# Kernel optimization log

Measured on AMD Instinct MI355X. Metric: run time of the kernel, lower is better.

Reference implementation:

```python
import jax, jax.numpy as jnp
import numpy as np

N_NODES = 50000

def _gcn_norm(edge_index, num_nodes):
    # add self-loops, compute symmetric normalization D^-1/2 (A+I) D^-1/2
    loops = jnp.arange(num_nodes, dtype=edge_index.dtype)
    row = jnp.concatenate([edge_index[0], loops])  # target nodes
    col = jnp.concatenate([edge_index[1], loops])  # source nodes
    deg = jax.ops.segment_sum(jnp.ones_like(row, dtype=jnp.float32), row, num_segments=num_nodes)
    dinv = jnp.where(deg > 0, 1.0 / jnp.sqrt(deg), 0.0)
    norm = dinv[row] * dinv[col]  # [E+N]
    return row, col, norm

def _gcn_layer(x, W, b, row, col, norm, num_nodes):
    h = x @ W  # [N, out] transform first (PyG GCNConv order)
    msg = h[col] * norm[:, None]  # gather sources, scale
    out = jax.ops.segment_sum(msg, row, num_segments=num_nodes)  # scatter-add to targets
    return out + b

def setup_inputs() -> dict:
    key = jax.random.key(0)
    ks = jax.random.split(key, 8)
    F_IN, HID, C = 512, 128, 40
    x = jax.random.normal(ks[0], (N_NODES, F_IN), dtype=jnp.float32)
    edge_index = jax.random.randint(ks[1], (2, 800000), 0, N_NODES, dtype=jnp.int32)
    W1 = jax.random.normal(ks[2], (F_IN, HID), dtype=jnp.float32) / np.sqrt(F_IN)
    b1 = jnp.zeros((HID,), dtype=jnp.float32)
    W2 = jax.random.normal(ks[3], (HID, HID), dtype=jnp.float32) / np.sqrt(HID)
    b2 = jnp.zeros((HID,), dtype=jnp.float32)
    W3 = jax.random.normal(ks[4], (HID, C), dtype=jnp.float32) / np.sqrt(HID)
    b3 = jnp.zeros((C,), dtype=jnp.float32)
    return {"x": x, "edge_index": edge_index, "W1": W1, "b1": b1, "W2": W2, "b2": b2, "W3": W3, "b3": b3}

def reference(x, edge_index, W1, b1, W2, b2, W3, b3):
    row, col, norm = _gcn_norm(edge_index, N_NODES)
    h = _gcn_layer(x, W1, b1, row, col, norm, N_NODES)
    h = jax.nn.relu(h)  # dropout is identity in eval mode
    h = _gcn_layer(h, W2, b2, row, col, norm, N_NODES)
    h = jax.nn.relu(h)
    h = _gcn_layer(h, W3, b3, row, col, norm, N_NODES)
    return jax.nn.log_softmax(h, axis=1)
```

## Files before the change

kernel.cpp:

```cpp
#include <hip/hip_runtime.h>
#include <hip/hip_bf16.h>
#include <math.h>

#define N_NODES 50000
#define N_EDGES 800000
#define F_IN 512
#define HID 128
#define NCLS 40
#define CAP 64
#define NBIN 8
#define BIN_SZ 6250

typedef unsigned short u16;
typedef __attribute__((ext_vector_type(8))) short short8;
typedef __attribute__((ext_vector_type(4))) float f32x4;

__device__ inline u16 f2bf(float f) {
    unsigned int u = __float_as_uint(f);
    unsigned int r = (u + 0x7FFFu + ((u >> 16) & 1u)) >> 16;
    return (u16)r;
}
__device__ inline float bf2f(u16 b) {
    return __uint_as_float(((unsigned int)b) << 16);
}


__global__ void k_zero_cnt(int* __restrict__ cnt) {
    int i = blockIdx.x * 256 + threadIdx.x;
    if (i < N_NODES) cnt[i] = 0;
}

__global__ void k_scatter_fx(const int* __restrict__ row, const int* __restrict__ col,
                             int* __restrict__ cnt, int* __restrict__ csr_col) {
    int bin = blockIdx.x & 7;
    int gblk = blockIdx.x >> 3;
    int nblk = gridDim.x >> 3;
    int lo = bin * BIN_SZ, hi = lo + BIN_SZ;
    for (int e = gblk * 256 + threadIdx.x; e < N_EDGES; e += nblk * 256) {
        int r = row[e];
        if (r >= lo && r < hi) {
            int pos = atomicAdd(&cnt[r], 1);
            if (pos < CAP) csr_col[(size_t)r * CAP + pos] = col[e];
        }
    }
}

__global__ void k_dinv_fx(int* __restrict__ cnt, float* __restrict__ dinv) {
    int i = blockIdx.x * 256 + threadIdx.x;
    if (i < N_NODES) {
        int d = cnt[i];
        if (d > CAP) { d = CAP; cnt[i] = CAP; }
        dinv[i] = rsqrtf((float)(d + 1));
    }
}

__global__ void k_nrm_fx(const int* __restrict__ cnt, const int* __restrict__ csr_col,
                         const float* __restrict__ dinv, float* __restrict__ csr_nrm) {
    int gid = blockIdx.x * 256 + threadIdx.x;
    if (gid >= N_NODES * CAP) return;
    int i = gid >> 6;
    int s = gid & (CAP - 1);
    if (s < cnt[i]) {
        int c = csr_col[(size_t)i * CAP + s];
        csr_nrm[(size_t)i * CAP + s] = dinv[i] * dinv[c];
    }
}


__global__ void k_wsplit(const float* __restrict__ W, u16* __restrict__ Whi, int Kdim) {
    int idx = blockIdx.x * 256 + threadIdx.x;
    if (idx >= Kdim * 128) return;
    int k = idx >> 7, n = idx & 127;
    u16 hb = f2bf(W[idx]);
    int s = k >> 5, hq = (k >> 3) & 3, q = k & 7;
    int j = n >> 4, lnn = n & 15;
    size_t pos = ((((size_t)s * 8 + j) * 16 + lnn) * 32) + hq * 8 + q;
    Whi[pos] = hb;
}


template<int K, bool AF32>
__device__ __forceinline__ void gemm_body(const void* __restrict__ Ap,
                                          const u16* __restrict__ Wh,
                                          u16* __restrict__ C, int M) {
    constexpr int NC = K / 64;
    constexpr int CH_BYTES = AF32 ? 8192 : 4096;
    __shared__ unsigned char sA[2][CH_BYTES];

    const int t = threadIdx.x;
    const int w = t >> 6, l = t & 63;
    const int ln = l & 15, h = l >> 4;
    const int row0 = blockIdx.x * 32;

    f32x4 acc[2][2];
    #pragma unroll
    for (int i = 0; i < 2; ++i)
        #pragma unroll
        for (int jj = 0; jj < 2; ++jj)
            acc[i][jj] = (f32x4){0.f, 0.f, 0.f, 0.f};

    auto stage = [&](int c, int buf) {
        if constexpr (AF32) {
            const float* X = (const float*)Ap;
            #pragma unroll
            for (int i = 0; i < 2; ++i) {
                int f = i * 256 + t;
                int r = f >> 4;
                int sub = f & 15;
                int srow = row0 + r; if (srow > M - 1) srow = M - 1;
                int colf = (sub * 4) ^ ((r & 7) << 3);
                const float* gp = X + (size_t)srow * K + c * 64 + colf;
                unsigned char* lp = &sA[buf][f * 16];
                __builtin_amdgcn_global_load_lds(
                    (const __attribute__((address_space(1))) void*)gp,
                    (__attribute__((address_space(3))) void*)lp, 16, 0, 0);
            }
        } else {
            const u16* X = (const u16*)Ap;
            int r = t >> 3;
            int sub = t & 7;
            int srow = row0 + r; if (srow > M - 1) srow = M - 1;
            int cole = (sub * 8) ^ ((r & 7) << 3);
            const u16* gp = X + (size_t)srow * K + c * 64 + cole;
            unsigned char* lp = &sA[buf][t * 16];
            __builtin_amdgcn_global_load_lds(
                (const __attribute__((address_space(1))) void*)gp,
                (__attribute__((address_space(3))) void*)lp, 16, 0, 0);
        }
    };

    stage(0, 0);
    __syncthreads();

    int buf = 0;
    for (int c = 0; c < NC; ++c) {
        short8 bh[2][2];
        #pragma unroll
        for (int s = 0; s < 2; ++s) {
            const int sg = c * 2 + s;
            #pragma unroll
            for (int jj = 0; jj < 2; ++jj) {
                size_t off = ((((size_t)sg * 8 + 2 * w + jj) * 16 + ln) * 32) + h * 8;
                bh[s][jj] = *(const short8*)(Wh + off);
            }
        }
        if (c + 1 < NC) stage(c + 1, buf ^ 1);

        short8 ah[2][2];
        if constexpr (AF32) {
            #pragma unroll
            for (int s = 0; s < 2; ++s)
                #pragma unroll
                for (int i = 0; i < 2; ++i) {
                    int rb = (i * 16 + ln) * 256;
                    int sw = (ln & 7) << 5;
                    int a0 = rb + ((s * 128 + h * 32) ^ sw);
                    float4 p0 = *(const float4*)&sA[buf][a0];
                    float4 p1 = *(const float4*)&sA[buf][a0 + 16];
                    union { short8 s8; u16 u[8]; } cv;
                    cv.u[0] = f2bf(p0.x); cv.u[1] = f2bf(p0.y);
                    cv.u[2] = f2bf(p0.z); cv.u[3] = f2bf(p0.w);
                    cv.u[4] = f2bf(p1.x); cv.u[5] = f2bf(p1.y);
                    cv.u[6] = f2bf(p1.z); cv.u[7] = f2bf(p1.w);
                    ah[s][i] = cv.s8;
                }
        } else {
            #pragma unroll
            for (int s = 0; s < 2; ++s)
                #pragma unroll
                for (int i = 0; i < 2; ++i) {
                    int rb = (i * 16 + ln) * 128;
                    int sw = (ln & 7) << 4;
                    ah[s][i] = *(const short8*)&sA[buf][rb + ((s * 64 + h * 16) ^ sw)];
                }
        }

        #pragma unroll
        for (int s = 0; s < 2; ++s)
            #pragma unroll
            for (int i = 0; i < 2; ++i)
                #pragma unroll
                for (int jj = 0; jj < 2; ++jj)
                    acc[i][jj] = __builtin_amdgcn_mfma_f32_16x16x32_bf16(
                        ah[s][i], bh[s][jj], acc[i][jj], 0, 0, 0);

        __syncthreads();
        buf ^= 1;
    }

    #pragma unroll
    for (int i = 0; i < 2; ++i)
        #pragma unroll
        for (int v = 0; v < 4; ++v) {
            int gr = row0 + i * 16 + h * 4 + v;
            if (gr < M) {
                #pragma unroll
                for (int jj = 0; jj < 2; ++jj)
                    __builtin_nontemporal_store(
                        f2bf(acc[i][jj][v]),
                        &C[(size_t)gr * 128 + w * 32 + jj * 16 + ln]);
            }
        }
}

__global__ __launch_bounds__(256) void k_gemmL1(const void* __restrict__ Ap,
                                                const u16* __restrict__ Wh,
                                                u16* __restrict__ C, int M) {
    gemm_body<F_IN, true>(Ap, Wh, C, M);
}

__global__ __launch_bounds__(256) void k_gemmL2(const void* __restrict__ Ap,
                                                const u16* __restrict__ Wh,
                                                u16* __restrict__ C, int M) {
    gemm_body<HID, false>(Ap, Wh, C, M);
}


__global__ void k_gemm40(const u16* __restrict__ A, const float* __restrict__ W,
                         u16* __restrict__ C, int M) {
    __shared__ float As[64][132];
    __shared__ float Ws[128][40];
    int t = threadIdx.x;
    int row0 = blockIdx.x * 64;
    #pragma unroll
    for (int i = 0; i < 4; ++i) {
        int fidx = t + i * 256;
        int r = fidx >> 4;
        int c = (fidx & 15) * 8;
        int gr = row0 + r;
        uint4 v = {0, 0, 0, 0};
        if (gr < M) v = *reinterpret_cast<const uint4*>(A + (size_t)gr * 128 + c);
        const u16* pv = (const u16*)&v;
        #pragma unroll
        for (int q = 0; q < 8; ++q) As[r][c + q] = bf2f(pv[q]);
    }
    #pragma unroll
    for (int i = 0; i < 5; ++i) {
        int fidx = t + i * 256;
        int r = fidx / 10, c = (fidx % 10) << 2;
        float4 v = *reinterpret_cast<const float4*>(W + r * 40 + c);
        *reinterpret_cast<float4*>(&Ws[r][c]) = v;
    }
    __syncthreads();
    int r = t >> 2;
    int cg = t & 3;
    float acc[10];
    #pragma unroll
    for (int j = 0; j < 10; ++j) acc[j] = 0.0f;
    for (int k = 0; k < 128; ++k) {
        float a = As[r][k];
        #pragma unroll
        for (int j = 0; j < 10; ++j)
            acc[j] = fmaf(a, Ws[k][cg * 10 + j], acc[j]);
    }
    int gr = row0 + r;
    if (gr < M) {
        u16* base = C + (size_t)gr * 40 + cg * 10;
        #pragma unroll
        for (int j = 0; j < 5; ++j) {
            unsigned int p = (unsigned int)f2bf(acc[2 * j]) |
                             ((unsigned int)f2bf(acc[2 * j + 1]) << 16);
            __builtin_nontemporal_store(p, (unsigned int*)(base + 2 * j));
        }
    }
}


__global__ void k_agg_csr_bf(const u16* __restrict__ h, const float* __restrict__ dinv,
                             const float* __restrict__ bias,
                             const int* __restrict__ cnt, const int* __restrict__ csr_col,
                             const float* __restrict__ csr_nrm, u16* __restrict__ out) {
    int gid = blockIdx.x * 256 + threadIdx.x;
    if (gid >= N_NODES * 32) return;
    int i = gid >> 5;
    int q = (gid & 31) * 4;
    const u16* hq = h + q;
    float di = dinv[i];
    float s = di * di;
    ushort4 hv = *reinterpret_cast<const ushort4*>(hq + (size_t)i * 128);
    float4 bv = *reinterpret_cast<const float4*>(bias + q);
    float4 acc;
    acc.x = fmaf(bf2f(hv.x), s, bv.x);
    acc.y = fmaf(bf2f(hv.y), s, bv.y);
    acc.z = fmaf(bf2f(hv.z), s, bv.z);
    acc.w = fmaf(bf2f(hv.w), s, bv.w);
    int e = (int)((size_t)i * CAP);
    int e1 = e + cnt[i];
    for (; e + 8 <= e1; e += 8) {
        int c0 = csr_col[e],     c1 = csr_col[e + 1], c2 = csr_col[e + 2], c3 = csr_col[e + 3];
        int c4 = csr_col[e + 4], c5 = csr_col[e + 5], c6 = csr_col[e + 6], c7 = csr_col[e + 7];
        float n0 = csr_nrm[e],     n1 = csr_nrm[e + 1], n2 = csr_nrm[e + 2], n3 = csr_nrm[e + 3];
        float n4 = csr_nrm[e + 4], n5 = csr_nrm[e + 5], n6 = csr_nrm[e + 6], n7 = csr_nrm[e + 7];
        ushort4 v0 = *reinterpret_cast<const ushort4*>(hq + (size_t)c0 * 128);
        ushort4 v1 = *reinterpret_cast<const ushort4*>(hq + (size_t)c1 * 128);
        ushort4 v2 = *reinterpret_cast<const ushort4*>(hq + (size_t)c2 * 128);
        ushort4 v3 = *reinterpret_cast<const ushort4*>(hq + (size_t)c3 * 128);
        ushort4 v4 = *reinterpret_cast<const ushort4*>(hq + (size_t)c4 * 128);
        ushort4 v5 = *reinterpret_cast<const ushort4*>(hq + (size_t)c5 * 128);
        ushort4 v6 = *reinterpret_cast<const ushort4*>(hq + (size_t)c6 * 128);
        ushort4 v7 = *reinterpret_cast<const ushort4*>(hq + (size_t)c7 * 128);
        acc.x = fmaf(bf2f(v0.x), n0, acc.x); acc.y = fmaf(bf2f(v0.y), n0, acc.y);
        acc.z = fmaf(bf2f(v0.z), n0, acc.z); acc.w = fmaf(bf2f(v0.w), n0, acc.w);
        acc.x = fmaf(bf2f(v1.x), n1, acc.x); acc.y = fmaf(bf2f(v1.y), n1, acc.y);
        acc.z = fmaf(bf2f(v1.z), n1, acc.z); acc.w = fmaf(bf2f(v1.w), n1, acc.w);
        acc.x = fmaf(bf2f(v2.x), n2, acc.x); acc.y = fmaf(bf2f(v2.y), n2, acc.y);
        acc.z = fmaf(bf2f(v2.z), n2, acc.z); acc.w = fmaf(bf2f(v2.w), n2, acc.w);
        acc.x = fmaf(bf2f(v3.x), n3, acc.x); acc.y = fmaf(bf2f(v3.y), n3, acc.y);
        acc.z = fmaf(bf2f(v3.z), n3, acc.z); acc.w = fmaf(bf2f(v3.w), n3, acc.w);
        acc.x = fmaf(bf2f(v4.x), n4, acc.x); acc.y = fmaf(bf2f(v4.y), n4, acc.y);
        acc.z = fmaf(bf2f(v4.z), n4, acc.z); acc.w = fmaf(bf2f(v4.w), n4, acc.w);
        acc.x = fmaf(bf2f(v5.x), n5, acc.x); acc.y = fmaf(bf2f(v5.y), n5, acc.y);
        acc.z = fmaf(bf2f(v5.z), n5, acc.z); acc.w = fmaf(bf2f(v5.w), n5, acc.w);
        acc.x = fmaf(bf2f(v6.x), n6, acc.x); acc.y = fmaf(bf2f(v6.y), n6, acc.y);
        acc.z = fmaf(bf2f(v6.z), n6, acc.z); acc.w = fmaf(bf2f(v6.w), n6, acc.w);
        acc.x = fmaf(bf2f(v7.x), n7, acc.x); acc.y = fmaf(bf2f(v7.y), n7, acc.y);
        acc.z = fmaf(bf2f(v7.z), n7, acc.z); acc.w = fmaf(bf2f(v7.w), n7, acc.w);
    }
    for (; e < e1; ++e) {
        int c0 = csr_col[e];
        float n0 = csr_nrm[e];
        ushort4 v0 = *reinterpret_cast<const ushort4*>(hq + (size_t)c0 * 128);
        acc.x = fmaf(bf2f(v0.x), n0, acc.x); acc.y = fmaf(bf2f(v0.y), n0, acc.y);
        acc.z = fmaf(bf2f(v0.z), n0, acc.z); acc.w = fmaf(bf2f(v0.w), n0, acc.w);
    }
    ushort4 o;
    o.x = f2bf(fmaxf(acc.x, 0.f));
    o.y = f2bf(fmaxf(acc.y, 0.f));
    o.z = f2bf(fmaxf(acc.z, 0.f));
    o.w = f2bf(fmaxf(acc.w, 0.f));
    *reinterpret_cast<ushort4*>(out + (size_t)i * 128 + q) = o;
}


__global__ void k_agg_csr40_bf(const u16* __restrict__ h, const float* __restrict__ dinv,
                               const float* __restrict__ bias,
                               const int* __restrict__ cnt, const int* __restrict__ csr_col,
                               const float* __restrict__ csr_nrm, float* __restrict__ out) {
    const int TPN = 10;
    int gid = blockIdx.x * 256 + threadIdx.x;
    if (gid >= N_NODES * TPN) return;
    int i = gid / TPN;
    int q = (gid % TPN) * 4;
    const u16* hq = h + q;
    float di = dinv[i];
    float s = di * di;
    ushort4 hv = *reinterpret_cast<const ushort4*>(hq + (size_t)i * 40);
    float4 bv = *reinterpret_cast<const float4*>(bias + q);
    float4 acc;
    acc.x = fmaf(bf2f(hv.x), s, bv.x);
    acc.y = fmaf(bf2f(hv.y), s, bv.y);
    acc.z = fmaf(bf2f(hv.z), s, bv.z);
    acc.w = fmaf(bf2f(hv.w), s, bv.w);
    int e = (int)((size_t)i * CAP);
    int e1 = e + cnt[i];
    for (; e + 4 <= e1; e += 4) {
        int c0 = csr_col[e], c1 = csr_col[e + 1], c2 = csr_col[e + 2], c3 = csr_col[e + 3];
        float n0 = csr_nrm[e], n1 = csr_nrm[e + 1], n2 = csr_nrm[e + 2], n3 = csr_nrm[e + 3];
        ushort4 v0 = *reinterpret_cast<const ushort4*>(hq + (size_t)c0 * 40);
        ushort4 v1 = *reinterpret_cast<const ushort4*>(hq + (size_t)c1 * 40);
        ushort4 v2 = *reinterpret_cast<const ushort4*>(hq + (size_t)c2 * 40);
        ushort4 v3 = *reinterpret_cast<const ushort4*>(hq + (size_t)c3 * 40);
        acc.x = fmaf(bf2f(v0.x), n0, acc.x); acc.y = fmaf(bf2f(v0.y), n0, acc.y);
        acc.z = fmaf(bf2f(v0.z), n0, acc.z); acc.w = fmaf(bf2f(v0.w), n0, acc.w);
        acc.x = fmaf(bf2f(v1.x), n1, acc.x); acc.y = fmaf(bf2f(v1.y), n1, acc.y);
        acc.z = fmaf(bf2f(v1.z), n1, acc.z); acc.w = fmaf(bf2f(v1.w), n1, acc.w);
        acc.x = fmaf(bf2f(v2.x), n2, acc.x); acc.y = fmaf(bf2f(v2.y), n2, acc.y);
        acc.z = fmaf(bf2f(v2.z), n2, acc.z); acc.w = fmaf(bf2f(v2.w), n2, acc.w);
        acc.x = fmaf(bf2f(v3.x), n3, acc.x); acc.y = fmaf(bf2f(v3.y), n3, acc.y);
        acc.z = fmaf(bf2f(v3.z), n3, acc.z); acc.w = fmaf(bf2f(v3.w), n3, acc.w);
    }
    for (; e < e1; ++e) {
        int c0 = csr_col[e];
        float n0 = csr_nrm[e];
        ushort4 v0 = *reinterpret_cast<const ushort4*>(hq + (size_t)c0 * 40);
        acc.x = fmaf(bf2f(v0.x), n0, acc.x); acc.y = fmaf(bf2f(v0.y), n0, acc.y);
        acc.z = fmaf(bf2f(v0.z), n0, acc.z); acc.w = fmaf(bf2f(v0.w), n0, acc.w);
    }
    *reinterpret_cast<float4*>(out + (size_t)i * 40 + q) = acc;
}


__global__ void k_logsoftmax(float* __restrict__ out) {
    int wave = threadIdx.x >> 6, lane = threadIdx.x & 63;
    int rowi = blockIdx.x * 4 + wave;
    if (rowi >= N_NODES) return;
    float v = (lane < NCLS) ? out[(size_t)rowi * NCLS + lane] : -INFINITY;
    float m = v;
    #pragma unroll
    for (int off = 32; off; off >>= 1) m = fmaxf(m, __shfl_xor(m, off));
    float ex = (lane < NCLS) ? expf(v - m) : 0.0f;
    float s = ex;
    #pragma unroll
    for (int off = 32; off; off >>= 1) s += __shfl_xor(s, off);
    float ls = logf(s);
    if (lane < NCLS) out[(size_t)rowi * NCLS + lane] = v - m - ls;
}


extern "C" void kernel_launch(void* const* d_in, const int* in_sizes, int n_in,
                              void* d_out, int out_size, void* d_ws, size_t ws_size,
                              hipStream_t stream) {
    const float* x  = (const float*)d_in[0];
    const int* ei   = (const int*)d_in[1];
    const float* W1 = (const float*)d_in[2];
    const float* b1 = (const float*)d_in[3];
    const float* W2 = (const float*)d_in[4];
    const float* b2 = (const float*)d_in[5];
    const float* W3 = (const float*)d_in[6];
    const float* b3 = (const float*)d_in[7];
    float* out = (float*)d_out;

    const int* row = ei;
    const int* col = ei + N_EDGES;

    char* ws = (char*)d_ws;
    int*   cnt     = (int*)ws;   ws += sizeof(int) * N_NODES;
    int*   csr_col = (int*)ws;   ws += sizeof(int) * (size_t)N_NODES * CAP;
    float* csr_nrm = (float*)ws; ws += sizeof(float) * (size_t)N_NODES * CAP;
    float* dinv    = (float*)ws; ws += sizeof(float) * N_NODES;
    u16*   wt1hi   = (u16*)ws;   ws += sizeof(u16) * F_IN * 128;
    u16*   wt2hi   = (u16*)ws;   ws += sizeof(u16) * HID * 128;
    u16*   hbuf    = (u16*)ws;   ws += sizeof(u16) * (size_t)N_NODES * HID;
    u16*   abuf    = (u16*)ws;   ws += sizeof(u16) * (size_t)N_NODES * HID;
    u16*   h3      = (u16*)ws;   ws += sizeof(u16) * (size_t)N_NODES * NCLS;

    const int NB_N   = (N_NODES + 255) / 256;
    const int NB_G   = (N_NODES + 63) / 64;
    const int NB_G32 = (N_NODES + 31) / 32;
    const int NB_BIN = 2048;
    const int NB_SLOT = (N_NODES * CAP + 255) / 256;

    k_wsplit<<<(F_IN * 128 + 255) / 256, 256, 0, stream>>>(W1, wt1hi, F_IN);
    k_wsplit<<<(HID * 128 + 255) / 256, 256, 0, stream>>>(W2, wt2hi, HID);

    k_zero_cnt<<<NB_N, 256, 0, stream>>>(cnt);
    k_scatter_fx<<<NB_BIN, 256, 0, stream>>>(row, col, cnt, csr_col);
    k_dinv_fx<<<NB_N, 256, 0, stream>>>(cnt, dinv);
    k_nrm_fx<<<NB_SLOT, 256, 0, stream>>>(cnt, csr_col, dinv, csr_nrm);

    k_gemmL1<<<NB_G32, 256, 0, stream>>>(x, wt1hi, hbuf, N_NODES);
    k_agg_csr_bf<<<(N_NODES * 32 + 255) / 256, 256, 0, stream>>>(
        hbuf, dinv, b1, cnt, csr_col, csr_nrm, abuf);

    k_gemmL2<<<NB_G32, 256, 0, stream>>>(abuf, wt2hi, hbuf, N_NODES);
    k_agg_csr_bf<<<(N_NODES * 32 + 255) / 256, 256, 0, stream>>>(
        hbuf, dinv, b2, cnt, csr_col, csr_nrm, abuf);

    k_gemm40<<<NB_G, 256, 0, stream>>>(abuf, W3, h3, N_NODES);
    k_agg_csr40_bf<<<(N_NODES * 10 + 255) / 256, 256, 0, stream>>>(
        h3, dinv, b3, cnt, csr_col, csr_nrm, out);
    k_logsoftmax<<<(N_NODES + 3) / 4, 256, 0, stream>>>(out);
}
```

Baseline: 220.9 us.

## Fuse prep kernels, fold dinv into consumers, fuse final aggregation with log-softmax

```diff
diff --git a/kernel.cpp b/kernel.cpp
--- a/kernel.cpp
+++ b/kernel.cpp
@@ -25,10 +25,28 @@
 }
 
 
-__global__ void k_zero_cnt(int* __restrict__ cnt) {
-    int i = blockIdx.x * 256 + threadIdx.x;
-    if (i < N_NODES) cnt[i] = 0;
-}
+__device__ inline void wsplit_one(const float* __restrict__ W, u16* __restrict__ Whi,
+                                  int idx, int Kdim) {
+    int k = idx >> 7, n = idx & 127;
+    u16 hb = f2bf(W[idx]);
+    int s = k >> 5, hq = (k >> 3) & 3, q = k & 7;
+    int j = n >> 4, lnn = n & 15;
+    size_t pos = ((((size_t)s * 8 + j) * 16 + lnn) * 32) + hq * 8 + q;
+    Whi[pos] = hb;
+}
+
+__global__ void k_prep(const float* __restrict__ W1, const float* __restrict__ W2,
+                       u16* __restrict__ wt1hi, u16* __restrict__ wt2hi,
+                       int* __restrict__ cnt) {
+    int idx = blockIdx.x * 256 + threadIdx.x;
+    if (idx < N_NODES) cnt[idx] = 0;
+    if (idx < F_IN * 128) {
+        wsplit_one(W1, wt1hi, idx, F_IN);
+    } else if (idx < F_IN * 128 + HID * 128) {
+        wsplit_one(W2, wt2hi, idx - F_IN * 128, HID);
+    }
+}
+
 
 __global__ void k_scatter_fx(const int* __restrict__ row, const int* __restrict__ col,
                              int* __restrict__ cnt, int* __restrict__ csr_col) {
@@ -45,37 +63,19 @@
     }
 }
 
-__global__ void k_dinv_fx(int* __restrict__ cnt, float* __restrict__ dinv) {
-    int i = blockIdx.x * 256 + threadIdx.x;
-    if (i < N_NODES) {
-        int d = cnt[i];
-        if (d > CAP) { d = CAP; cnt[i] = CAP; }
-        dinv[i] = rsqrtf((float)(d + 1));
-    }
-}
-
 __global__ void k_nrm_fx(const int* __restrict__ cnt, const int* __restrict__ csr_col,
-                         const float* __restrict__ dinv, float* __restrict__ csr_nrm) {
+                         float* __restrict__ csr_nrm) {
     int gid = blockIdx.x * 256 + threadIdx.x;
     if (gid >= N_NODES * CAP) return;
     int i = gid >> 6;
     int s = gid & (CAP - 1);
-    if (s < cnt[i]) {
+    int d = min(cnt[i], CAP);
+    if (s < d) {
         int c = csr_col[(size_t)i * CAP + s];
-        csr_nrm[(size_t)i * CAP + s] = dinv[i] * dinv[c];
-    }
-}
-
-
-__global__ void k_wsplit(const float* __restrict__ W, u16* __restrict__ Whi, int Kdim) {
-    int idx = blockIdx.x * 256 + threadIdx.x;
-    if (idx >= Kdim * 128) return;
-    int k = idx >> 7, n = idx & 127;
-    u16 hb = f2bf(W[idx]);
-    int s = k >> 5, hq = (k >> 3) & 3, q = k & 7;
-    int j = n >> 4, lnn = n & 15;
-    size_t pos = ((((size_t)s * 8 + j) * 16 + lnn) * 32) + hq * 8 + q;
-    Whi[pos] = hb;
+        int dc = min(cnt[c], CAP);
+        csr_nrm[(size_t)i * CAP + s] =
+            rsqrtf((float)(d + 1)) * rsqrtf((float)(dc + 1));
+    }
 }
 
 
@@ -266,8 +266,7 @@
 }
 
 
-__global__ void k_agg_csr_bf(const u16* __restrict__ h, const float* __restrict__ dinv,
-                             const float* __restrict__ bias,
+__global__ void k_agg_csr_bf(const u16* __restrict__ h, const float* __restrict__ bias,
                              const int* __restrict__ cnt, const int* __restrict__ csr_col,
                              const float* __restrict__ csr_nrm, u16* __restrict__ out) {
     int gid = blockIdx.x * 256 + threadIdx.x;
@@ -275,7 +274,8 @@
     int i = gid >> 5;
     int q = (gid & 31) * 4;
     const u16* hq = h + q;
-    float di = dinv[i];
+    int d = min(cnt[i], CAP);
+    float di = rsqrtf((float)(d + 1));
     float s = di * di;
     ushort4 hv = *reinterpret_cast<const ushort4*>(hq + (size_t)i * 128);
     float4 bv = *reinterpret_cast<const float4*>(bias + q);
@@ -285,7 +285,7 @@
     acc.z = fmaf(bf2f(hv.z), s, bv.z);
     acc.w = fmaf(bf2f(hv.w), s, bv.w);
     int e = (int)((size_t)i * CAP);
-    int e1 = e + cnt[i];
+    int e1 = e + d;
     for (; e + 8 <= e1; e += 8) {
         int c0 = csr_col[e],     c1 = csr_col[e + 1], c2 = csr_col[e + 2], c3 = csr_col[e + 3];
         int c4 = csr_col[e + 4], c5 = csr_col[e + 5], c6 = csr_col[e + 6], c7 = csr_col[e + 7];
@@ -332,68 +332,76 @@
 }
 
 
-__global__ void k_agg_csr40_bf(const u16* __restrict__ h, const float* __restrict__ dinv,
-                               const float* __restrict__ bias,
-                               const int* __restrict__ cnt, const int* __restrict__ csr_col,
-                               const float* __restrict__ csr_nrm, float* __restrict__ out) {
-    const int TPN = 10;
-    int gid = blockIdx.x * 256 + threadIdx.x;
-    if (gid >= N_NODES * TPN) return;
-    int i = gid / TPN;
-    int q = (gid % TPN) * 4;
-    const u16* hq = h + q;
-    float di = dinv[i];
-    float s = di * di;
-    ushort4 hv = *reinterpret_cast<const ushort4*>(hq + (size_t)i * 40);
-    float4 bv = *reinterpret_cast<const float4*>(bias + q);
-    float4 acc;
-    acc.x = fmaf(bf2f(hv.x), s, bv.x);
-    acc.y = fmaf(bf2f(hv.y), s, bv.y);
-    acc.z = fmaf(bf2f(hv.z), s, bv.z);
-    acc.w = fmaf(bf2f(hv.w), s, bv.w);
-    int e = (int)((size_t)i * CAP);
-    int e1 = e + cnt[i];
-    for (; e + 4 <= e1; e += 4) {
-        int c0 = csr_col[e], c1 = csr_col[e + 1], c2 = csr_col[e + 2], c3 = csr_col[e + 3];
-        float n0 = csr_nrm[e], n1 = csr_nrm[e + 1], n2 = csr_nrm[e + 2], n3 = csr_nrm[e + 3];
-        ushort4 v0 = *reinterpret_cast<const ushort4*>(hq + (size_t)c0 * 40);
-        ushort4 v1 = *reinterpret_cast<const ushort4*>(hq + (size_t)c1 * 40);
-        ushort4 v2 = *reinterpret_cast<const ushort4*>(hq + (size_t)c2 * 40);
-        ushort4 v3 = *reinterpret_cast<const ushort4*>(hq + (size_t)c3 * 40);
-        acc.x = fmaf(bf2f(v0.x), n0, acc.x); acc.y = fmaf(bf2f(v0.y), n0, acc.y);
-        acc.z = fmaf(bf2f(v0.z), n0, acc.z); acc.w = fmaf(bf2f(v0.w), n0, acc.w);
-        acc.x = fmaf(bf2f(v1.x), n1, acc.x); acc.y = fmaf(bf2f(v1.y), n1, acc.y);
-        acc.z = fmaf(bf2f(v1.z), n1, acc.z); acc.w = fmaf(bf2f(v1.w), n1, acc.w);
-        acc.x = fmaf(bf2f(v2.x), n2, acc.x); acc.y = fmaf(bf2f(v2.y), n2, acc.y);
-        acc.z = fmaf(bf2f(v2.z), n2, acc.z); acc.w = fmaf(bf2f(v2.w), n2, acc.w);
-        acc.x = fmaf(bf2f(v3.x), n3, acc.x); acc.y = fmaf(bf2f(v3.y), n3, acc.y);
-        acc.z = fmaf(bf2f(v3.z), n3, acc.z); acc.w = fmaf(bf2f(v3.w), n3, acc.w);
-    }
-    for (; e < e1; ++e) {
-        int c0 = csr_col[e];
-        float n0 = csr_nrm[e];
-        ushort4 v0 = *reinterpret_cast<const ushort4*>(hq + (size_t)c0 * 40);
-        acc.x = fmaf(bf2f(v0.x), n0, acc.x); acc.y = fmaf(bf2f(v0.y), n0, acc.y);
-        acc.z = fmaf(bf2f(v0.z), n0, acc.z); acc.w = fmaf(bf2f(v0.w), n0, acc.w);
-    }
-    *reinterpret_cast<float4*>(out + (size_t)i * 40 + q) = acc;
-}
-
-
-__global__ void k_logsoftmax(float* __restrict__ out) {
-    int wave = threadIdx.x >> 6, lane = threadIdx.x & 63;
-    int rowi = blockIdx.x * 4 + wave;
-    if (rowi >= N_NODES) return;
-    float v = (lane < NCLS) ? out[(size_t)rowi * NCLS + lane] : -INFINITY;
-    float m = v;
-    #pragma unroll
-    for (int off = 32; off; off >>= 1) m = fmaxf(m, __shfl_xor(m, off));
-    float ex = (lane < NCLS) ? expf(v - m) : 0.0f;
-    float s = ex;
-    #pragma unroll
-    for (int off = 32; off; off >>= 1) s += __shfl_xor(s, off);
-    float ls = logf(s);
-    if (lane < NCLS) out[(size_t)rowi * NCLS + lane] = v - m - ls;
+__global__ void k_agg40_ls(const u16* __restrict__ h, const float* __restrict__ bias,
+                           const int* __restrict__ cnt, const int* __restrict__ csr_col,
+                           const float* __restrict__ csr_nrm, float* __restrict__ out) {
+    __shared__ float sv[25][44];
+    __shared__ float sm[25], sl[25];
+    int t = threadIdx.x;
+    int nd = t / 10;
+    int q = (t % 10) * 4;
+    int i = blockIdx.x * 25 + nd;
+    bool act = (t < 250) && (i < N_NODES);
+    float4 acc = make_float4(0.f, 0.f, 0.f, 0.f);
+    if (act) {
+        const u16* hq = h + q;
+        int d = min(cnt[i], CAP);
+        float di = rsqrtf((float)(d + 1));
+        float s = di * di;
+        ushort4 hv = *reinterpret_cast<const ushort4*>(hq + (size_t)i * 40);
+        float4 bv = *reinterpret_cast<const float4*>(bias + q);
+        acc.x = fmaf(bf2f(hv.x), s, bv.x);
+        acc.y = fmaf(bf2f(hv.y), s, bv.y);
+        acc.z = fmaf(bf2f(hv.z), s, bv.z);
+        acc.w = fmaf(bf2f(hv.w), s, bv.w);
+        int e = (int)((size_t)i * CAP);
+        int e1 = e + d;
+        for (; e + 4 <= e1; e += 4) {
+            int c0 = csr_col[e], c1 = csr_col[e + 1], c2 = csr_col[e + 2], c3 = csr_col[e + 3];
+            float n0 = csr_nrm[e], n1 = csr_nrm[e + 1], n2 = csr_nrm[e + 2], n3 = csr_nrm[e + 3];
+            ushort4 v0 = *reinterpret_cast<const ushort4*>(hq + (size_t)c0 * 40);
+            ushort4 v1 = *reinterpret_cast<const ushort4*>(hq + (size_t)c1 * 40);
+            ushort4 v2 = *reinterpret_cast<const ushort4*>(hq + (size_t)c2 * 40);
+            ushort4 v3 = *reinterpret_cast<const ushort4*>(hq + (size_t)c3 * 40);
+            acc.x = fmaf(bf2f(v0.x), n0, acc.x); acc.y = fmaf(bf2f(v0.y), n0, acc.y);
+            acc.z = fmaf(bf2f(v0.z), n0, acc.z); acc.w = fmaf(bf2f(v0.w), n0, acc.w);
+            acc.x = fmaf(bf2f(v1.x), n1, acc.x); acc.y = fmaf(bf2f(v1.y), n1, acc.y);
+            acc.z = fmaf(bf2f(v1.z), n1, acc.z); acc.w = fmaf(bf2f(v1.w), n1, acc.w);
+            acc.x = fmaf(bf2f(v2.x), n2, acc.x); acc.y = fmaf(bf2f(v2.y), n2, acc.y);
+            acc.z = fmaf(bf2f(v2.z), n2, acc.z); acc.w = fmaf(bf2f(v2.w), n2, acc.w);
+            acc.x = fmaf(bf2f(v3.x), n3, acc.x); acc.y = fmaf(bf2f(v3.y), n3, acc.y);
+            acc.z = fmaf(bf2f(v3.z), n3, acc.z); acc.w = fmaf(bf2f(v3.w), n3, acc.w);
+        }
+        for (; e < e1; ++e) {
+            int c0 = csr_col[e];
+            float n0 = csr_nrm[e];
+            ushort4 v0 = *reinterpret_cast<const ushort4*>(hq + (size_t)c0 * 40);
+            acc.x = fmaf(bf2f(v0.x), n0, acc.x); acc.y = fmaf(bf2f(v0.y), n0, acc.y);
+            acc.z = fmaf(bf2f(v0.z), n0, acc.z); acc.w = fmaf(bf2f(v0.w), n0, acc.w);
+        }
+        sv[nd][q + 0] = acc.x;
+        sv[nd][q + 1] = acc.y;
+        sv[nd][q + 2] = acc.z;
+        sv[nd][q + 3] = acc.w;
+    }
+    __syncthreads();
+    if (t < 25 && blockIdx.x * 25 + t < N_NODES) {
+        float m = -INFINITY;
+        #pragma unroll 8
+        for (int f = 0; f < NCLS; ++f) m = fmaxf(m, sv[t][f]);
+        float ssum = 0.f;
+        #pragma unroll 8
+        for (int f = 0; f < NCLS; ++f) ssum += expf(sv[t][f] - m);
+        sm[t] = m;
+        sl[t] = logf(ssum);
+    }
+    __syncthreads();
+    if (act) {
+        float m = sm[nd], ls = sl[nd];
+        float4 o = make_float4(acc.x - m - ls, acc.y - m - ls,
+                               acc.z - m - ls, acc.w - m - ls);
+        *reinterpret_cast<float4*>(out + (size_t)i * 40 + q) = o;
+    }
 }
 
 
@@ -417,37 +425,32 @@
     int*   cnt     = (int*)ws;   ws += sizeof(int) * N_NODES;
     int*   csr_col = (int*)ws;   ws += sizeof(int) * (size_t)N_NODES * CAP;
     float* csr_nrm = (float*)ws; ws += sizeof(float) * (size_t)N_NODES * CAP;
-    float* dinv    = (float*)ws; ws += sizeof(float) * N_NODES;
     u16*   wt1hi   = (u16*)ws;   ws += sizeof(u16) * F_IN * 128;
     u16*   wt2hi   = (u16*)ws;   ws += sizeof(u16) * HID * 128;
     u16*   hbuf    = (u16*)ws;   ws += sizeof(u16) * (size_t)N_NODES * HID;
     u16*   abuf    = (u16*)ws;   ws += sizeof(u16) * (size_t)N_NODES * HID;
     u16*   h3      = (u16*)ws;   ws += sizeof(u16) * (size_t)N_NODES * NCLS;
 
-    const int NB_N   = (N_NODES + 255) / 256;
-    const int NB_G   = (N_NODES + 63) / 64;
-    const int NB_G32 = (N_NODES + 31) / 32;
-    const int NB_BIN = 2048;
+    const int NB_G    = (N_NODES + 63) / 64;
+    const int NB_G32  = (N_NODES + 31) / 32;
+    const int NB_BIN  = 2048;
     const int NB_SLOT = (N_NODES * CAP + 255) / 256;
-
-    k_wsplit<<<(F_IN * 128 + 255) / 256, 256, 0, stream>>>(W1, wt1hi, F_IN);
-    k_wsplit<<<(HID * 128 + 255) / 256, 256, 0, stream>>>(W2, wt2hi, HID);
-
-    k_zero_cnt<<<NB_N, 256, 0, stream>>>(cnt);
+    const int NB_PREP = ((F_IN + HID) * 128 + 255) / 256;
+
+    k_prep<<<NB_PREP, 256, 0, stream>>>(W1, W2, wt1hi, wt2hi, cnt);
+
     k_scatter_fx<<<NB_BIN, 256, 0, stream>>>(row, col, cnt, csr_col);
-    k_dinv_fx<<<NB_N, 256, 0, stream>>>(cnt, dinv);
-    k_nrm_fx<<<NB_SLOT, 256, 0, stream>>>(cnt, csr_col, dinv, csr_nrm);
+    k_nrm_fx<<<NB_SLOT, 256, 0, stream>>>(cnt, csr_col, csr_nrm);
 
     k_gemmL1<<<NB_G32, 256, 0, stream>>>(x, wt1hi, hbuf, N_NODES);
     k_agg_csr_bf<<<(N_NODES * 32 + 255) / 256, 256, 0, stream>>>(
-        hbuf, dinv, b1, cnt, csr_col, csr_nrm, abuf);
+        hbuf, b1, cnt, csr_col, csr_nrm, abuf);
 
     k_gemmL2<<<NB_G32, 256, 0, stream>>>(abuf, wt2hi, hbuf, N_NODES);
     k_agg_csr_bf<<<(N_NODES * 32 + 255) / 256, 256, 0, stream>>>(
-        hbuf, dinv, b2, cnt, csr_col, csr_nrm, abuf);
+        hbuf, b2, cnt, csr_col, csr_nrm, abuf);
 
     k_gemm40<<<NB_G, 256, 0, stream>>>(abuf, W3, h3, N_NODES);
-    k_agg_csr40_bf<<<(N_NODES * 10 + 255) / 256, 256, 0, stream>>>(
-        h3, dinv, b3, cnt, csr_col, csr_nrm, out);
-    k_logsoftmax<<<(N_NODES + 3) / 4, 256, 0, stream>>>(out);
-}
+    k_agg40_ls<<<(N_NODES + 24) / 25, 256, 0, stream>>>(
+        h3, b3, cnt, csr_col, csr_nrm, out);
+}
```

Result: no change. 223.4 us (+1.1%).
